# Kernel optimization log

Hardware: AMD Instinct MI355X
Metric: run time of the kernel (lower is better)

The kernel has to match this reference:

```python
import jax, jax.numpy as jnp
import numpy as np

B, S, H = 8, 2048, 4096
REFRACTORY_STEPS = 5.0


def setup_inputs() -> dict:
    key = jax.random.key(0)
    kx, = jax.random.split(key, 1)
    x = jax.random.normal(kx, (B, S, H), dtype=jnp.float32)
    membrane_threshold = jnp.float32(0.5)  # nn.Parameter(torch.tensor(threshold))
    decay_rate = jnp.float32(0.95)         # nn.Parameter(torch.tensor(decay))
    return {"x": x, "membrane_threshold": membrane_threshold, "decay_rate": decay_rate}


def reference(x, membrane_threshold, decay_rate):
    # LIF spiking scan over time. State: membrane potential + refractory counter, each [B,H].
    b, s, h = x.shape
    dt = x.dtype

    def step(carry, x_t):
        mem, ref = carry
        mem = decay_rate * mem + x_t                      # leaky integrate
        ref = jnp.maximum(ref - 1.0, 0.0)                 # clamp(ref-1, min=0)
        can_spike = (ref == 0.0)
        spk = (can_spike & (mem > membrane_threshold)).astype(dt)
        mem = mem * (1.0 - spk)                           # reset on spike
        ref = ref + spk * REFRACTORY_STEPS                # enter refractory period
        return (mem, ref), spk

    init = (jnp.zeros((b, h), dt), jnp.zeros((b, h), dt))
    xs = jnp.swapaxes(x, 0, 1)                            # [S,B,H] for scan over time
    _, spikes = jax.lax.scan(step, init, xs)              # spikes: [S,B,H]
    return jnp.swapaxes(spikes, 0, 1)                     # [B,S,H]
```

## Files before the change

### kernel.cpp

```cpp
#include <hip/hip_runtime.h>
#include <stdint.h>


#define S_LEN 2048
#define H_DIM 4096
#define TS 64
#define NT (S_LEN / TS)

typedef __attribute__((address_space(3))) uint32_t lds_u32;
typedef __attribute__((address_space(1))) const uint32_t gbl_u32;
typedef float f32x4 __attribute__((ext_vector_type(4)));

__global__ __launch_bounds__(128, 1) void lif_kernel(
    const float* __restrict__ x,
    const float* __restrict__ thr_p,
    const float* __restrict__ decay_p,
    float* __restrict__ out)
{
    __shared__ __attribute__((aligned(16))) float xbuf[3][TS][64];
    __shared__ __attribute__((aligned(16))) float obuf[2][TS][64];

    const int lane = threadIdx.x & 63;
    const int wid  = threadIdx.x >> 6;
    const int b    = blockIdx.x >> 6;
    const int h0   = (blockIdx.x & 63) * 64;
    const size_t seq_base = (size_t)b * S_LEN * H_DIM;

    if (wid == 1) {
        const int lrow = lane >> 4;
        const int lcol = (lane & 15) * 4;
        const float* gsrc0 = x   + seq_base + (size_t)lrow * H_DIM + h0 + lcol;
        float*       gdst0 = out + seq_base + (size_t)lrow * H_DIM + h0 + lcol;

        asm volatile("s_waitcnt vmcnt(0) lgkmcnt(0)" ::: "memory");

        auto issue_tile = [&](int t, int buf) {
            const float* g = gsrc0 + (size_t)t * TS * H_DIM;
#pragma unroll
            for (int k = 0; k < 16; ++k) {
                __builtin_amdgcn_global_load_lds(
                    (gbl_u32*)(g + (size_t)k * 4 * H_DIM),
                    (lds_u32*)&xbuf[buf][k * 4][0],
                    16, 0, 0);
            }
        };
        auto flush_tile = [&](int t) {
            float*       gd   = gdst0 + (size_t)t * TS * H_DIM;
            const float* lsrc = &obuf[t & 1][0][0];
#pragma unroll
            for (int k = 0; k < 16; ++k) {
                const f32x4 v = *(const f32x4*)(lsrc + k * 256 + lane * 4);
                __builtin_nontemporal_store(v, (f32x4*)(gd + (size_t)k * 4 * H_DIM));
            }
        };

        issue_tile(0, 0);
        issue_tile(1, 1);

        for (int t = 0; t < NT; ++t) {
            if (t <= 1)                     asm volatile("s_waitcnt vmcnt(16)" ::: "memory");
            else if (t == 2 || t == NT - 1) asm volatile("s_waitcnt vmcnt(32)" ::: "memory");
            else                            asm volatile("s_waitcnt vmcnt(48)" ::: "memory");

            asm volatile("s_barrier" ::: "memory");

            if (t + 2 < NT) issue_tile(t + 2, (t + 2) % 3);
            if (t >= 1)     flush_tile(t - 1);
        }

        asm volatile("s_barrier" ::: "memory");
        flush_tile(NT - 1);
    } else {
        const float thr   = thr_p[0];
        const float decay = decay_p[0];

        float mem = 0.0f;
        float ref = 0.0f;

        for (int t = 0; t < NT; ++t) {
            asm volatile("s_barrier" ::: "memory");

            const float* xb = &xbuf[t % 3][0][0];
            float*       ob = &obuf[t & 1][0][0];
#pragma unroll
            for (int s = 0; s < TS; ++s) {
                const float xv   = xb[s * 64 + lane];
                const float memn = __fadd_rn(__fmul_rn(decay, mem), xv);
                ref = fmaxf(__fadd_rn(ref, -1.0f), 0.0f);
                const bool spk_b = (ref == 0.0f) & (memn > thr);
                mem = spk_b ? 0.0f : memn;
                ref = __fadd_rn(ref, spk_b ? 5.0f : 0.0f);
                ob[s * 64 + lane] = spk_b ? 1.0f : 0.0f;
            }
            asm volatile("s_waitcnt lgkmcnt(0)" ::: "memory");
        }
        asm volatile("s_barrier" ::: "memory");
    }
}

extern "C" void kernel_launch(void* const* d_in, const int* in_sizes, int n_in,
                              void* d_out, int out_size, void* d_ws, size_t ws_size,
                              hipStream_t stream) {
    const float* x     = (const float*)d_in[0];
    const float* thr   = (const float*)d_in[1];
    const float* decay = (const float*)d_in[2];
    float*       out   = (float*)d_out;

    lif_kernel<<<dim3(512), dim3(128), 0, stream>>>(x, thr, decay, out);
}
```

Measured before the change: 81.02 us.

## Split load and store into separate waves; precompute decayed membrane

```diff
diff --git a/kernel.cpp b/kernel.cpp
--- a/kernel.cpp
+++ b/kernel.cpp
@@ -11,7 +11,7 @@
 typedef __attribute__((address_space(1))) const uint32_t gbl_u32;
 typedef float f32x4 __attribute__((ext_vector_type(4)));
 
-__global__ __launch_bounds__(128, 1) void lif_kernel(
+__global__ __launch_bounds__(192, 1) void lif_kernel(
     const float* __restrict__ x,
     const float* __restrict__ thr_p,
     const float* __restrict__ decay_p,
@@ -29,8 +29,7 @@
     if (wid == 1) {
         const int lrow = lane >> 4;
         const int lcol = (lane & 15) * 4;
-        const float* gsrc0 = x   + seq_base + (size_t)lrow * H_DIM + h0 + lcol;
-        float*       gdst0 = out + seq_base + (size_t)lrow * H_DIM + h0 + lcol;
+        const float* gsrc0 = x + seq_base + (size_t)lrow * H_DIM + h0 + lcol;
 
         asm volatile("s_waitcnt vmcnt(0) lgkmcnt(0)" ::: "memory");
 
@@ -44,6 +43,22 @@
                     16, 0, 0);
             }
         };
+
+        issue_tile(0, 0);
+        issue_tile(1, 1);
+
+        for (int t = 0; t < NT; ++t) {
+            if (t == NT - 1) asm volatile("s_waitcnt vmcnt(0)"  ::: "memory");
+            else             asm volatile("s_waitcnt vmcnt(16)" ::: "memory");
+            asm volatile("s_barrier" ::: "memory");
+            if (t + 2 < NT) issue_tile(t + 2, (t + 2) % 3);
+        }
+        asm volatile("s_barrier" ::: "memory");
+    } else if (wid == 2) {
+        const int lrow = lane >> 4;
+        const int lcol = (lane & 15) * 4;
+        float* gdst0 = out + seq_base + (size_t)lrow * H_DIM + h0 + lcol;
+
         auto flush_tile = [&](int t) {
             float*       gd   = gdst0 + (size_t)t * TS * H_DIM;
             const float* lsrc = &obuf[t & 1][0][0];
@@ -54,43 +69,36 @@
             }
         };
 
-        issue_tile(0, 0);
-        issue_tile(1, 1);
-
         for (int t = 0; t < NT; ++t) {
-            if (t <= 1)                     asm volatile("s_waitcnt vmcnt(16)" ::: "memory");
-            else if (t == 2 || t == NT - 1) asm volatile("s_waitcnt vmcnt(32)" ::: "memory");
-            else                            asm volatile("s_waitcnt vmcnt(48)" ::: "memory");
-
             asm volatile("s_barrier" ::: "memory");
-
-            if (t + 2 < NT) issue_tile(t + 2, (t + 2) % 3);
-            if (t >= 1)     flush_tile(t - 1);
+            if (t >= 1) {
+                flush_tile(t - 1);
+                asm volatile("s_waitcnt lgkmcnt(0)" ::: "memory");
+            }
         }
-
         asm volatile("s_barrier" ::: "memory");
         flush_tile(NT - 1);
     } else {
         const float thr   = thr_p[0];
         const float decay = decay_p[0];
 
-        float mem = 0.0f;
-        float ref = 0.0f;
+        float dmem = 0.0f;
+        float ref  = 0.0f;
 
         for (int t = 0; t < NT; ++t) {
             asm volatile("s_barrier" ::: "memory");
-
             const float* xb = &xbuf[t % 3][0][0];
             float*       ob = &obuf[t & 1][0][0];
 #pragma unroll
             for (int s = 0; s < TS; ++s) {
                 const float xv   = xb[s * 64 + lane];
-                const float memn = __fadd_rn(__fmul_rn(decay, mem), xv);
-                ref = fmaxf(__fadd_rn(ref, -1.0f), 0.0f);
-                const bool spk_b = (ref == 0.0f) & (memn > thr);
-                mem = spk_b ? 0.0f : memn;
-                ref = __fadd_rn(ref, spk_b ? 5.0f : 0.0f);
-                ob[s * 64 + lane] = spk_b ? 1.0f : 0.0f;
+                const float memn = __fadd_rn(dmem, xv);
+                const float refm = fmaxf(__fadd_rn(ref, -1.0f), 0.0f);
+                const bool  spk  = (refm == 0.0f) & (memn > thr);
+                const float dm   = __fmul_rn(decay, memn);
+                dmem = spk ? 0.0f : dm;
+                ref  = __fadd_rn(refm, spk ? 5.0f : 0.0f);
+                ob[s * 64 + lane] = spk ? 1.0f : 0.0f;
             }
             asm volatile("s_waitcnt lgkmcnt(0)" ::: "memory");
         }
@@ -106,5 +114,5 @@
     const float* decay = (const float*)d_in[2];
     float*       out   = (float*)d_out;
 
-    lif_kernel<<<dim3(512), dim3(128), 0, stream>>>(x, thr, decay, out);
+    lif_kernel<<<dim3(512), dim3(192), 0, stream>>>(x, thr, decay, out);
 }
```

After: 82.47 us. No clear change (+1.8%).
